# Kernel tuning notes

Measured on AMD Instinct MI355X. Metric: run time of the kernel, lower is better.

## Reference

```python
import jax, jax.numpy as jnp
import numpy as np

B, S, HID = 2, 2048, 2048
H, KV, D = 16, 8, 128
EPS = 1e-6


def _rope_embeds(B, S, D):
    # standard RoPE cos/sin table, concatenated along last dim: [B, S, D]
    pos = jnp.arange(S, dtype=jnp.float32)  # same positions per batch row
    inv_freq = 1.0 / (10000.0 ** (jnp.arange(0, D // 2, dtype=jnp.float32) * (2.0 / D)))
    ang = pos[:, None] * inv_freq[None, :]  # [S, D/2]
    pe = jnp.concatenate([jnp.cos(ang), jnp.sin(ang)], axis=-1)  # [S, D]
    return jnp.broadcast_to(pe[None], (B, S, D))


def setup_inputs() -> dict:
    key = jax.random.key(0)
    ks = jax.random.split(key, 5)
    scale = 0.02
    return {
        "x": jax.random.normal(ks[0], (B, S, HID), jnp.float32),
        "pos_embeds": _rope_embeds(B, S, D),
        "q_w": jax.random.normal(ks[1], (H * D, HID), jnp.float32) * scale,
        "k_w": jax.random.normal(ks[2], (KV * D, HID), jnp.float32) * scale,
        "v_w": jax.random.normal(ks[3], (KV * D, HID), jnp.float32) * scale,
        "o_w": jax.random.normal(ks[4], (HID, H * D), jnp.float32) * scale,
        "q_norm_w": jnp.ones((D,), jnp.float32),
        "k_norm_w": jnp.ones((D,), jnp.float32),
    }


def _rmsnorm(x, w):
    var = jnp.mean(jnp.square(x), axis=-1, keepdims=True)
    return x * jax.lax.rsqrt(var + EPS) * w


def _apply_rope(x, pos_embeds):
    # x: [B, S, h, D]; pos_embeds: [B, S, D] = cat(cos, sin)
    x1, x2 = jnp.split(x, 2, axis=-1)
    cos, sin = jnp.split(pos_embeds[:, :, None, :], 2, axis=-1)
    return jnp.concatenate([x1 * cos - x2 * sin, x1 * sin + x2 * cos], axis=-1)


def reference(x, pos_embeds, q_w, k_w, v_w, o_w, q_norm_w, k_norm_w):
    b, s, _ = x.shape
    q = _apply_rope(_rmsnorm((x @ q_w.T).reshape(b, s, H, D), q_norm_w), pos_embeds)
    k = _apply_rope(_rmsnorm((x @ k_w.T).reshape(b, s, KV, D), k_norm_w), pos_embeds)
    v = (x @ v_w.T).reshape(b, s, KV, D)
    # GQA: repeat kv heads to match query heads
    rep = H // KV
    k = jnp.repeat(k, rep, axis=2)
    v = jnp.repeat(v, rep, axis=2)
    scores = jnp.einsum("bqhd,bkhd->bhqk", q, k) * (1.0 / np.sqrt(D))
    causal = jnp.tril(jnp.ones((s, s), dtype=bool))
    scores = jnp.where(causal[None, None], scores, jnp.finfo(scores.dtype).min)
    attn = jax.nn.softmax(scores, axis=-1)
    out = jnp.einsum("bhqk,bkhd->bqhd", attn, v).reshape(b, s, H * D)
    return out @ o_w.T
```

## Files before the change

kernel.cpp:

```cpp
#include <hip/hip_runtime.h>
#include <hip/hip_bf16.h>

#define BATCH 2
#define SEQ   2048
#define HID   2048
#define NH    16
#define NKV   8
#define HD    128

typedef __bf16 bf16;
typedef bf16  bf16x8  __attribute__((ext_vector_type(8)));
typedef bf16  bf16x4  __attribute__((ext_vector_type(4)));
typedef float floatx4 __attribute__((ext_vector_type(4)));

typedef __attribute__((address_space(3))) void lds_void;
typedef const __attribute__((address_space(1))) void gmem_void;

__device__ inline void async16(const void* g, void* l) {
    __builtin_amdgcn_global_load_lds((gmem_void*)g, (lds_void*)l, 16, 0, 0);
}

#define XN  8388608u
#define QWN 4194304u
#define KWN 2097152u
#define VWN 2097152u
#define OWN 4194304u

__global__ __launch_bounds__(256) void cvt_all(bf16* __restrict__ dst,
                                               const float* __restrict__ x,
                                               const float* __restrict__ qw,
                                               const float* __restrict__ kw,
                                               const float* __restrict__ vw,
                                               const float* __restrict__ ow)
{
    const int blk = blockIdx.x;
    const float* src;
    size_t off;
    if (blk < 4096)      { src = x;  off = (size_t)blk * 2048; }
    else if (blk < 6144) { src = qw; off = (size_t)(blk - 4096) * 2048; }
    else if (blk < 7168) { src = kw; off = (size_t)(blk - 6144) * 2048; }
    else if (blk < 8192) { src = vw; off = (size_t)(blk - 7168) * 2048; }
    else                 { src = ow; off = (size_t)(blk - 8192) * 2048; }

    const int t = threadIdx.x * 8;
    const float4* p = (const float4*)(src + off + t);
    float4 u0 = p[0], u1 = p[1];
    bf16x8 v;
    v[0] = (bf16)u0.x; v[1] = (bf16)u0.y; v[2] = (bf16)u0.z; v[3] = (bf16)u0.w;
    v[4] = (bf16)u1.x; v[5] = (bf16)u1.y; v[6] = (bf16)u1.z; v[7] = (bf16)u1.w;
    *(bf16x8*)(dst + (size_t)blk * 2048 + t) = v;
}

template <int AMODE, int WMODE, int CMODE>
__global__ __launch_bounds__(256) void gemm128(void* __restrict__ Cp,
                                               const void* __restrict__ Ap,
                                               const void* __restrict__ Wp,
                                               int M, int N, int K)
{
    __shared__ bf16 As[128 * 64];
    __shared__ bf16 Ws[128 * 64];

    const int tid  = threadIdx.x;
    const int wv   = tid >> 6;
    const int lane = tid & 63;
    const int quad = lane >> 4;
    const int c    = lane & 15;

    const int nwg = gridDim.x * gridDim.y;
    int bx = blockIdx.x, by = blockIdx.y;
    if ((nwg & 7) == 0) {
        int lin = by * gridDim.x + bx;
        lin = (lin & 7) * (nwg >> 3) + (lin >> 3);
        bx = lin % gridDim.x;
        by = lin / gridDim.x;
    }
    const int m0 = bx * 128;
    const int n0 = by * 128;
    const int wm = (wv >> 1) * 64;
    const int wn = (wv & 1) * 64;

    const int arow = lane >> 3;
    const int acol = (lane & 7) * 8;

    floatx4 acc[4][4] = {};

    for (int k0 = 0; k0 < K; k0 += 64) {
        if constexpr (AMODE == 0) {
            const float* A = (const float*)Ap;
            #pragma unroll
            for (int it = 0; it < 4; it++) {
                int row = it * 32 + (tid >> 3);
                int col = (tid & 7) * 8;
                const float4* p = (const float4*)(A + (size_t)(m0 + row) * K + k0 + col);
                float4 u0 = p[0], u1 = p[1];
                bf16x8 v;
                v[0] = (bf16)u0.x; v[1] = (bf16)u0.y; v[2] = (bf16)u0.z; v[3] = (bf16)u0.w;
                v[4] = (bf16)u1.x; v[5] = (bf16)u1.y; v[6] = (bf16)u1.z; v[7] = (bf16)u1.w;
                *(bf16x8*)(&As[row * 64 + col]) = v;
            }
        } else {
            const bf16* A = (const bf16*)Ap;
            #pragma unroll
            for (int ch = 0; ch < 4; ch++) {
                int row = wv * 32 + ch * 8 + arow;
                async16(A + (size_t)(m0 + row) * K + k0 + acol,
                        &As[(wv * 32 + ch * 8) * 64]);
            }
        }
        if constexpr (WMODE == 0) {
            const float* W = (const float*)Wp;
            #pragma unroll
            for (int it = 0; it < 4; it++) {
                int row = it * 32 + (tid >> 3);
                int col = (tid & 7) * 8;
                const float4* p = (const float4*)(W + (size_t)(n0 + row) * K + k0 + col);
                float4 u0 = p[0], u1 = p[1];
                bf16x8 v;
                v[0] = (bf16)u0.x; v[1] = (bf16)u0.y; v[2] = (bf16)u0.z; v[3] = (bf16)u0.w;
                v[4] = (bf16)u1.x; v[5] = (bf16)u1.y; v[6] = (bf16)u1.z; v[7] = (bf16)u1.w;
                *(bf16x8*)(&Ws[row * 64 + col]) = v;
            }
        } else {
            const bf16* W = (const bf16*)Wp;
            #pragma unroll
            for (int ch = 0; ch < 4; ch++) {
                int row = wv * 32 + ch * 8 + arow;
                async16(W + (size_t)(n0 + row) * K + k0 + acol,
                        &Ws[(wv * 32 + ch * 8) * 64]);
            }
        }
        __syncthreads();

        #pragma unroll
        for (int t = 0; t < 2; t++) {
            bf16x8 af[4], bw[4];
            #pragma unroll
            for (int i = 0; i < 4; i++)
                af[i] = *(const bf16x8*)(&As[(wm + i * 16 + c) * 64 + t * 32 + quad * 8]);
            #pragma unroll
            for (int j = 0; j < 4; j++)
                bw[j] = *(const bf16x8*)(&Ws[(wn + j * 16 + c) * 64 + t * 32 + quad * 8]);
            #pragma unroll
            for (int i = 0; i < 4; i++)
                #pragma unroll
                for (int j = 0; j < 4; j++)
                    acc[i][j] = __builtin_amdgcn_mfma_f32_16x16x32_bf16(af[i], bw[j], acc[i][j], 0, 0, 0);
        }
        __syncthreads();
    }

    if constexpr (CMODE == 0) {
        float* C = (float*)Cp;
        #pragma unroll
        for (int i = 0; i < 4; i++)
            #pragma unroll
            for (int j = 0; j < 4; j++)
                #pragma unroll
                for (int r = 0; r < 4; r++) {
                    int m = m0 + wm + i * 16 + quad * 4 + r;
                    int n = n0 + wn + j * 16 + c;
                    C[(size_t)m * N + n] = acc[i][j][r];
                }
    } else if constexpr (CMODE == 1) {
        bf16* C = (bf16*)Cp;
        #pragma unroll
        for (int i = 0; i < 4; i++)
            #pragma unroll
            for (int j = 0; j < 4; j++)
                #pragma unroll
                for (int r = 0; r < 4; r++) {
                    int m = m0 + wm + i * 16 + quad * 4 + r;
                    int n = n0 + wn + j * 16 + c;
                    C[(size_t)m * N + n] = (bf16)acc[i][j][r];
                }
    } else if constexpr (CMODE == 2) {
        bf16* C = (bf16*)Cp;
        const int b = m0 >> 11;
        #pragma unroll
        for (int j = 0; j < 4; j++) {
            int n = n0 + wn + j * 16 + c;
            size_t base = ((size_t)b * N + n) * 2048;
            #pragma unroll
            for (int i = 0; i < 4; i++) {
                int s0 = (m0 & 2047) + wm + i * 16 + quad * 4;
                bf16x4 v;
                #pragma unroll
                for (int r = 0; r < 4; r++) v[r] = (bf16)acc[i][j][r];
                *(bf16x4*)(&C[base + s0]) = v;
            }
        }
    } else {
        bf16* Cq = (bf16*)Cp;
        if (n0 < 2048) {
            #pragma unroll
            for (int i = 0; i < 4; i++)
                #pragma unroll
                for (int j = 0; j < 4; j++)
                    #pragma unroll
                    for (int r = 0; r < 4; r++) {
                        int m = m0 + wm + i * 16 + quad * 4 + r;
                        int n = n0 + wn + j * 16 + c;
                        Cq[(size_t)m * 2048 + n] = (bf16)acc[i][j][r];
                    }
        } else if (n0 < 3072) {
            bf16* Ck = Cq + XN;
            #pragma unroll
            for (int i = 0; i < 4; i++)
                #pragma unroll
                for (int j = 0; j < 4; j++)
                    #pragma unroll
                    for (int r = 0; r < 4; r++) {
                        int m = m0 + wm + i * 16 + quad * 4 + r;
                        int n = n0 - 2048 + wn + j * 16 + c;
                        Ck[(size_t)m * 1024 + n] = (bf16)acc[i][j][r];
                    }
        } else {
            bf16* Cv = Cq + XN + QWN;
            const int b = m0 >> 11;
            #pragma unroll
            for (int j = 0; j < 4; j++) {
                int n = n0 - 3072 + wn + j * 16 + c;
                size_t base = ((size_t)b * 1024 + n) * 2048;
                #pragma unroll
                for (int i = 0; i < 4; i++) {
                    int s0 = (m0 & 2047) + wm + i * 16 + quad * 4;
                    bf16x4 v;
                    #pragma unroll
                    for (int r = 0; r < 4; r++) v[r] = (bf16)acc[i][j][r];
                    *(bf16x4*)(&Cv[base + s0]) = v;
                }
            }
        }
    }
}

__global__ __launch_bounds__(128) void norm_rope_k(bf16* __restrict__ k,
                                                   const float* __restrict__ pe,
                                                   const float* __restrict__ knw)
{
    const int s  = blockIdx.x;
    const int hh = blockIdx.y;
    const int b  = blockIdx.z;
    const int d  = threadIdx.x;

    bf16* buf = k + (size_t)(b * SEQ + s) * 1024 + hh * HD;

    float x = (float)buf[d];
    float ss = x * x;
    #pragma unroll
    for (int m = 32; m; m >>= 1) ss += __shfl_xor(ss, m);

    __shared__ float red[2];
    __shared__ float nv[128];
    if ((d & 63) == 0) red[d >> 6] = ss;
    __syncthreads();
    float var = (red[0] + red[1]) * (1.0f / 128.0f);
    float nx = x * rsqrtf(var + 1e-6f) * knw[d];
    nv[d] = nx;
    __syncthreads();

    const float* pev = pe + ((size_t)b * SEQ + s) * HD;
    float o;
    if (d < 64) {
        o = nx * pev[d] - nv[d + 64] * pev[64 + d];
    } else {
        o = nv[d - 64] * pev[d] + nx * pev[d - 64];
    }
    buf[d] = (bf16)o;
}

__global__ __launch_bounds__(512) void fattn(bf16* __restrict__ O,
                                             const bf16* __restrict__ Q,
                                             const bf16* __restrict__ Kh,
                                             const bf16* __restrict__ Vtg,
                                             const float* __restrict__ pe,
                                             const float* __restrict__ qnw)
{
    const int h    = blockIdx.z;
    const int b    = blockIdx.y;
    const int qblk = (h & 8) ? (int)blockIdx.x
                             : ((int)gridDim.x - 1 - (int)blockIdx.x);
    const int kv   = h >> 1;

    const int tid  = threadIdx.x;
    const int wv   = tid >> 6;
    const int lane = tid & 63;
    const int quad = lane >> 4;
    const int c    = lane & 15;

    __shared__ bf16 Ks[64 * 136];
    __shared__ bf16 Vs[128 * 72];
    __shared__ bf16 Ps[8 * 16 * 72];

    const int qw = qblk * 128 + wv * 16;

    bf16x8 qf[4];
    {
        const bf16* qp = Q + (size_t)(b * SEQ + qw + c) * 2048 + h * HD + quad * 8;
        float qv[4][8];
        float ss = 0.0f;
        #pragma unroll
        for (int t = 0; t < 4; t++) {
            bf16x8 raw = *(const bf16x8*)(qp + t * 32);
            #pragma unroll
            for (int j = 0; j < 8; j++) { qv[t][j] = (float)raw[j]; ss += qv[t][j] * qv[t][j]; }
        }
        ss += __shfl_xor(ss, 16);
        ss += __shfl_xor(ss, 32);
        const float inv = rsqrtf(ss * (1.0f / 128.0f) + 1e-6f);
        const float* pev = pe + (size_t)(b * SEQ + qw + c) * HD + quad * 8;
        float nx[4][8], pv[4][8];
        #pragma unroll
        for (int t = 0; t < 4; t++)
            #pragma unroll
            for (int j = 0; j < 8; j++) {
                pv[t][j] = pev[t * 32 + j];
                nx[t][j] = qv[t][j] * inv * qnw[t * 32 + quad * 8 + j];
            }
        #pragma unroll
        for (int t = 0; t < 2; t++)
            #pragma unroll
            for (int j = 0; j < 8; j++) {
                qf[t][j]     = (bf16)(nx[t][j] * pv[t][j]     - nx[t + 2][j] * pv[t + 2][j]);
                qf[t + 2][j] = (bf16)(nx[t][j] * pv[t + 2][j] + nx[t + 2][j] * pv[t][j]);
            }
    }

    floatx4 o_acc[8] = {};
    float l_part[4] = {};

    const bf16* kbase = Kh  + (size_t)b * SEQ * 1024 + kv * HD;
    const bf16* vbase = Vtg + ((size_t)b * 1024 + kv * HD) * 2048;

    const int kr  = tid >> 3, ksc = (tid & 7) * 16;
    const int vd  = tid >> 2, vkc = (tid & 3) * 16;
    bf16* psw = &Ps[wv * 16 * 72];
    const int nkt = 2 * qblk + 2;
    const float kS = 0.08838834764831845f * 1.4426950408889634f;
    const float kB = 11.5f * 1.4426950408889634f;

    bf16x8 kreg[2], vreg[2];
    {
        const bf16* kp = kbase + (size_t)kr * 1024 + ksc;
        const bf16* vp = vbase + (size_t)vd * 2048 + vkc;
        kreg[0] = *(const bf16x8*)(kp);
        kreg[1] = *(const bf16x8*)(kp + 8);
        vreg[0] = *(const bf16x8*)(vp);
        vreg[1] = *(const bf16x8*)(vp + 8);
    }

    for (int kt = 0; kt < nkt; kt++) {
        const int k0 = kt * 64;
        *(bf16x8*)(&Ks[kr * 136 + ksc])     = kreg[0];
        *(bf16x8*)(&Ks[kr * 136 + ksc + 8]) = kreg[1];
        *(bf16x8*)(&Vs[vd * 72 + vkc])      = vreg[0];
        *(bf16x8*)(&Vs[vd * 72 + vkc + 8])  = vreg[1];
        __syncthreads();

        if (kt + 1 < nkt) {
            const bf16* kp = kbase + (size_t)(k0 + 64 + kr) * 1024 + ksc;
            const bf16* vp = vbase + (size_t)vd * 2048 + (k0 + 64) + vkc;
            kreg[0] = *(const bf16x8*)(kp);
            kreg[1] = *(const bf16x8*)(kp + 8);
            vreg[0] = *(const bf16x8*)(vp);
            vreg[1] = *(const bf16x8*)(vp + 8);
        }

        if (k0 <= qw + 15) {
            floatx4 sc[4] = {};
            #pragma unroll
            for (int t = 0; t < 4; t++) {
                #pragma unroll
                for (int g = 0; g < 4; g++) {
                    bf16x8 kf = *(const bf16x8*)(&Ks[(g * 16 + c) * 136 + t * 32 + quad * 8]);
                    sc[g] = __builtin_amdgcn_mfma_f32_16x16x32_bf16(qf[t], kf, sc[g], 0, 0, 0);
                }
            }

            const bool tail = (kt >= nkt - 2);
            #pragma unroll
            for (int r = 0; r < 4; r++) {
                const int qrow = qw + quad * 4 + r;
                #pragma unroll
                for (int g = 0; g < 4; g++) {
                    float p = exp2f(sc[g][r] * kS - kB);
                    if (tail && (k0 + g * 16 + c > qrow)) p = 0.0f;
                    l_part[r] += p;
                    psw[(quad * 4 + r) * 72 + g * 16 + c] = (bf16)p;
                }
            }
            asm volatile("s_waitcnt lgkmcnt(0)" ::: "memory");
            bf16x8 pf0 = *(const bf16x8*)(&psw[c * 72 + quad * 8]);
            bf16x8 pf1 = *(const bf16x8*)(&psw[c * 72 + 32 + quad * 8]);

            #pragma unroll
            for (int f = 0; f < 8; f++) {
                bf16x8 vf0 = *(const bf16x8*)(&Vs[(f * 16 + c) * 72 + quad * 8]);
                bf16x8 vf1 = *(const bf16x8*)(&Vs[(f * 16 + c) * 72 + 32 + quad * 8]);
                o_acc[f] = __builtin_amdgcn_mfma_f32_16x16x32_bf16(pf0, vf0, o_acc[f], 0, 0, 0);
                o_acc[f] = __builtin_amdgcn_mfma_f32_16x16x32_bf16(pf1, vf1, o_acc[f], 0, 0, 0);
            }
        }
        __syncthreads();
    }

    #pragma unroll
    for (int r = 0; r < 4; r++) {
        float l = l_part[r];
        #pragma unroll
        for (int msk = 8; msk; msk >>= 1) l += __shfl_xor(l, msk);
        const float inv = 1.0f / l;
        bf16* op = O + (size_t)(b * SEQ + qw + quad * 4 + r) * 2048 + h * HD;
        #pragma unroll
        for (int f = 0; f < 8; f++) op[f * 16 + c] = (bf16)(o_acc[f][r] * inv);
    }
}

extern "C" void kernel_launch(void* const* d_in, const int* in_sizes, int n_in,
                              void* d_out, int out_size, void* d_ws, size_t ws_size,
                              hipStream_t stream)
{
    const float* x   = (const float*)d_in[0];
    const float* pe  = (const float*)d_in[1];
    const float* qw  = (const float*)d_in[2];
    const float* kw  = (const float*)d_in[3];
    const float* vw  = (const float*)d_in[4];
    const float* ow  = (const float*)d_in[5];
    const float* qnw = (const float*)d_in[6];
    const float* knw = (const float*)d_in[7];
    float* out = (float*)d_out;

    bf16* qb = (bf16*)d_ws;
    bf16* kb = qb + XN;
    bf16* vt = kb + KWN * 2;
    bf16* ab = vt + VWN * 2;
    bf16* cvt_base = ab + XN;

    const bool fit = ws_size >= (size_t)92274688;
    const int M = BATCH * SEQ;

    if (fit) {
        bf16* xb  = cvt_base;
        bf16* qwb = xb  + XN;
        bf16* owb = qwb + QWN + KWN + VWN;

        cvt_all<<<10240, 256, 0, stream>>>(xb, x, qw, kw, vw, ow);

        gemm128<1, 1, 3><<<dim3(32, 32), 256, 0, stream>>>(qb, xb, qwb, M, 4096, 2048);

        norm_rope_k<<<dim3(SEQ, NKV, BATCH), 128, 0, stream>>>(kb, pe, knw);
        fattn<<<dim3(SEQ / 128, BATCH, NH), 512, 0, stream>>>(ab, qb, kb, vt, pe, qnw);

        gemm128<1, 1, 0><<<dim3(32, 16), 256, 0, stream>>>(out, ab, owb, M, 2048, 2048);
    } else {
        gemm128<0, 0, 1><<<dim3(32, 16), 256, 0, stream>>>(qb, x, qw, M, 2048, 2048);
        gemm128<0, 0, 1><<<dim3(32,  8), 256, 0, stream>>>(kb, x, kw, M, 1024, 2048);
        gemm128<0, 0, 2><<<dim3(32,  8), 256, 0, stream>>>(vt, x, vw, M, 1024, 2048);

        norm_rope_k<<<dim3(SEQ, NKV, BATCH), 128, 0, stream>>>(kb, pe, knw);
        fattn<<<dim3(SEQ / 128, BATCH, NH), 512, 0, stream>>>(ab, qb, kb, vt, pe, qnw);

        gemm128<0, 0, 0><<<dim3(32, 16), 256, 0, stream>>>(out, ab, ow, M, 2048, 2048);
    }
}
```

Measured before the change: 373.1 us.

## Replace fused QKV GEMM with 256x256 double-buffered tile kernel

Adds a dedicated QKV projection GEMM that uses 256x256 output tiles with 512 threads. It double-buffers LDS via async global-to-LDS loads and remaps blocks for locality. Larger tiles raise arithmetic intensity and cut redundant global reads, and the prefetch of the next K-slice overlaps loads with MFMA work. The cost is 128 KB of LDS per block, only 256 blocks launched, and heavy accumulator register pressure, which lower occupancy and may cause spills.

```diff
diff --git a/kernel.cpp b/kernel.cpp
--- a/kernel.cpp
+++ b/kernel.cpp
@@ -51,6 +51,120 @@
     *(bf16x8*)(dst + (size_t)blk * 2048 + t) = v;
 }
 
+__global__ __launch_bounds__(512) void gemm256_qkv(bf16* __restrict__ Cq,
+                                                   const bf16* __restrict__ A,
+                                                   const bf16* __restrict__ W)
+{
+    __shared__ bf16 As[2 * 256 * 64];
+    __shared__ bf16 Ws[2 * 256 * 64];
+
+    const int tid  = threadIdx.x;
+    const int wv   = tid >> 6;
+    const int lane = tid & 63;
+    const int quad = lane >> 4;
+    const int c    = lane & 15;
+
+    int lin = blockIdx.y * gridDim.x + blockIdx.x;
+    lin = (lin & 7) * 32 + (lin >> 3);
+    const int m0 = (lin & 15) * 256;
+    const int n0 = (lin >> 4) * 256;
+
+    const int wm = (wv >> 2) * 128;
+    const int wn = (wv & 3) * 64;
+
+    const int srow = tid >> 3;
+    const int scol = (tid & 7) * 8;
+
+    constexpr int K  = 2048;
+    constexpr int NT = K / 64;
+
+    floatx4 acc[8][4] = {};
+
+    auto stage = [&](int kt, int sel) {
+        const size_t ko = (size_t)kt * 64;
+        bf16* Ab = &As[sel * 16384];
+        bf16* Wb = &Ws[sel * 16384];
+        #pragma unroll
+        for (int l = 0; l < 4; ++l)
+            async16(A + (size_t)(m0 + l * 64 + srow) * K + ko + scol,
+                    Ab + l * 4096 + wv * 512);
+        #pragma unroll
+        for (int l = 0; l < 4; ++l)
+            async16(W + (size_t)(n0 + l * 64 + srow) * K + ko + scol,
+                    Wb + l * 4096 + wv * 512);
+    };
+
+    stage(0, 0);
+
+    int sel = 0;
+    for (int t = 0; t < NT; ++t) {
+        __syncthreads();
+        if (t + 1 < NT) stage(t + 1, sel ^ 1);
+
+        const bf16* Ab = &As[sel * 16384];
+        const bf16* Wb = &Ws[sel * 16384];
+        #pragma unroll
+        for (int ks = 0; ks < 2; ++ks) {
+            bf16x8 af[8], bw[4];
+            #pragma unroll
+            for (int i = 0; i < 8; i++)
+                af[i] = *(const bf16x8*)(Ab + (wm + i * 16 + c) * 64 + ks * 32 + quad * 8);
+            #pragma unroll
+            for (int j = 0; j < 4; j++)
+                bw[j] = *(const bf16x8*)(Wb + (wn + j * 16 + c) * 64 + ks * 32 + quad * 8);
+            __builtin_amdgcn_s_setprio(1);
+            #pragma unroll
+            for (int i = 0; i < 8; i++)
+                #pragma unroll
+                for (int j = 0; j < 4; j++)
+                    acc[i][j] = __builtin_amdgcn_mfma_f32_16x16x32_bf16(af[i], bw[j], acc[i][j], 0, 0, 0);
+            __builtin_amdgcn_s_setprio(0);
+        }
+        sel ^= 1;
+    }
+
+    const int b = m0 >> 11;
+    if (n0 < 2048) {
+        #pragma unroll
+        for (int i = 0; i < 8; i++)
+            #pragma unroll
+            for (int j = 0; j < 4; j++)
+                #pragma unroll
+                for (int r = 0; r < 4; r++) {
+                    int m = m0 + wm + i * 16 + quad * 4 + r;
+                    int n = n0 + wn + j * 16 + c;
+                    Cq[(size_t)m * 2048 + n] = (bf16)acc[i][j][r];
+                }
+    } else if (n0 < 3072) {
+        bf16* Ck = Cq + XN;
+        #pragma unroll
+        for (int i = 0; i < 8; i++)
+            #pragma unroll
+            for (int j = 0; j < 4; j++)
+                #pragma unroll
+                for (int r = 0; r < 4; r++) {
+                    int m = m0 + wm + i * 16 + quad * 4 + r;
+                    int n = n0 - 2048 + wn + j * 16 + c;
+                    Ck[(size_t)m * 1024 + n] = (bf16)acc[i][j][r];
+                }
+    } else {
+        bf16* Cv = Cq + XN + QWN;
+        #pragma unroll
+        for (int j = 0; j < 4; j++) {
+            int n = n0 - 3072 + wn + j * 16 + c;
+            size_t base = ((size_t)b * 1024 + n) * 2048;
+            #pragma unroll
+            for (int i = 0; i < 8; i++) {
+                int s0 = (m0 & 2047) + wm + i * 16 + quad * 4;
+                bf16x4 v;
+                #pragma unroll
+                for (int r = 0; r < 4; r++) v[r] = (bf16)acc[i][j][r];
+                *(bf16x4*)(&Cv[base + s0]) = v;
+            }
+        }
+    }
+}
+
 template <int AMODE, int WMODE, int CMODE>
 __global__ __launch_bounds__(256) void gemm128(void* __restrict__ Cp,
                                                const void* __restrict__ Ap,
@@ -446,7 +560,7 @@
 
         cvt_all<<<10240, 256, 0, stream>>>(xb, x, qw, kw, vw, ow);
 
-        gemm128<1, 1, 3><<<dim3(32, 32), 256, 0, stream>>>(qb, xb, qwb, M, 4096, 2048);
+        gemm256_qkv<<<dim3(16, 16), 512, 0, stream>>>(qb, xb, qwb);
 
         norm_rope_k<<<dim3(SEQ, NKV, BATCH), 128, 0, stream>>>(kb, pe, knw);
         fattn<<<dim3(SEQ / 128, BATCH, NH), 512, 0, stream>>>(ab, qb, kb, vt, pe, qnw);
```

New measurement: 359.4 us. -3.7%, faster.
